# Optimization experiments

Hardware: AMD Instinct MI355X
Metric: run time of the kernel (lower is better)

The kernel has to match this reference:

```python
import jax, jax.numpy as jnp
import numpy as np

BATCH = 8
HIDDEN = 256          # per-head size == input channels
NUM_HEADS = 9
H_IMG = 48
W_IMG = 48


def make_R(w, h):
    """Relative-position feature tensor R[i,j,k,l] = [dx, dy, dx^2, dy^2, dx*dy]
    with dx = k - i, dy = l - j (matches torch.meshgrid indexing='ij')."""
    gx, gy = jnp.meshgrid(jnp.arange(w), jnp.arange(h), indexing='ij')
    grid = jnp.stack([gx, gy], axis=-1).astype(jnp.float32)        # (w,h,2)
    rel = grid[None, None, :, :, :] - grid[:, :, None, None, :]    # (w,h,w,h,2)
    return jnp.concatenate(
        [rel, rel ** 2, (rel[..., 0] * rel[..., 1])[..., None]], axis=-1
    )                                                              # (w,h,w,h,5)


def setup_inputs() -> dict:
    key = jax.random.key(0)
    k1, k2, k3, k4, k5 = jax.random.split(key, 5)
    hidden_states = jax.random.normal(k1, (BATCH, HIDDEN, H_IMG, W_IMG), dtype=jnp.float32)
    # init per module: centers ~ N(0, init_mu_std=2.0), spreads = 1 + N(0, 0.01)
    attention_centers = 2.0 * jax.random.normal(k2, (NUM_HEADS, 2), dtype=jnp.float32)
    attention_spreads = 1.0 + 0.01 * jax.random.normal(k3, (NUM_HEADS,), dtype=jnp.float32)
    value_w = 0.02 * jax.random.normal(k4, (HIDDEN, NUM_HEADS * HIDDEN), dtype=jnp.float32)
    value_b = 0.02 * jax.random.normal(k5, (HIDDEN,), dtype=jnp.float32)
    return {
        'hidden_states': hidden_states,
        'attention_centers': attention_centers,
        'attention_spreads': attention_spreads,
        'value_w': value_w,
        'value_b': value_b,
    }


def reference(hidden_states, attention_centers, attention_spreads, value_w, value_b):
    b, c, h, w = hidden_states.shape
    x = jnp.transpose(hidden_states, (0, 3, 2, 1))  # (b, w, h, c)

    # heads target vectors (isotropic gaussian): a = c = sigma^2, b = 0
    a = attention_spreads ** 2                       # (H,)
    mu1 = attention_centers[:, 0]
    mu2 = attention_centers[:, 1]
    # t_h = -1/2 * [-2 a mu1, -2 a mu2, a, a, 0] = [a mu1, a mu2, -a/2, -a/2, 0]
    u = jnp.stack([a * mu1, a * mu2, -0.5 * a, -0.5 * a, jnp.zeros_like(a)], axis=-1)  # (H,5)

    R = make_R(w, h)                                               # (w,h,w,h,5)
    scores = jnp.einsum('ijkld,hd->ijhkl', R, u)                   # (w,h,H,w,h)
    probs = jax.nn.softmax(scores.reshape(w, h, NUM_HEADS, -1), axis=-1)
    probs = probs.reshape(w, h, NUM_HEADS, w, h)
    # dropout is identity in eval mode

    vals = jnp.einsum('ijhkl,bkld->bijhd', probs, x)               # (b,w,h,H,c)
    vals = vals.reshape(b, w, h, NUM_HEADS * c)
    out = vals @ value_w.T + value_b                               # (b,w,h,hidden)
    out = jnp.transpose(out, (0, 3, 2, 1))                         # (b,hidden,h,w)
    return out, probs
```

## Files before the change

### kernel.cpp

```cpp
#include <hip/hip_runtime.h>
#include <cstdint>
#include <cstddef>

#define NHEAD 9
#define CHN   256
#define NB    8
#define WH    48
#define SS    2304
#define OUT0  4718592

typedef short bf16x8 __attribute__((ext_vector_type(8)));
typedef float f32x4  __attribute__((ext_vector_type(4)));

__device__ __forceinline__ float bf2f(unsigned int u16) {
    union { unsigned int i; float f; } v; v.i = u16 << 16; return v.f;
}
__device__ __forceinline__ unsigned short f2bf(float f) {
    union { float f; unsigned int i; } v; v.f = f;
    unsigned int x = v.i;
    unsigned int r = x + 0x7fffu + ((x >> 16) & 1u);
    return (unsigned short)(r >> 16);
}

__global__ __launch_bounds__(64) void k_pinit(const float* __restrict__ centers,
                                              const float* __restrict__ spreads,
                                              float* __restrict__ p1, float* __restrict__ p2,
                                              unsigned short* __restrict__ p1b,
                                              unsigned short* __restrict__ p2b) {
    int blk = blockIdx.x;
    int h = blk / 48, r = blk % 48;
    int lane = threadIdx.x;
    float a = spreads[h]; a = a * a;
    float mu1 = centers[2 * h + 0];
    float mu2 = centers[2 * h + 1];
    bool act = lane < 48;
    float dx = (float)(lane - r);
    float q  = -0.5f * a * dx * dx;
    float g1 = act ? (a * mu1 * dx + q) : -INFINITY;
    float g2 = act ? (a * mu2 * dx + q) : -INFINITY;
    float m1 = g1, m2 = g2;
    #pragma unroll
    for (int off = 32; off >= 1; off >>= 1) {
        m1 = fmaxf(m1, __shfl_xor(m1, off));
        m2 = fmaxf(m2, __shfl_xor(m2, off));
    }
    float e1 = act ? expf(g1 - m1) : 0.f;
    float e2 = act ? expf(g2 - m2) : 0.f;
    float s1 = e1, s2 = e2;
    #pragma unroll
    for (int off = 32; off >= 1; off >>= 1) {
        s1 += __shfl_xor(s1, off);
        s2 += __shfl_xor(s2, off);
    }
    float v1 = e1 / s1, v2 = e2 / s2;
    if (act) {
        p1[h * SS + r * 48 + lane] = v1;
        p2[h * SS + r * 48 + lane] = v2;
    }
    p1b[(h * 48 + r) * 64 + lane] = act ? f2bf(v1) : 0;
    p2b[(h * 48 + r) * 64 + lane] = act ? f2bf(v2) : 0;
}

__global__ __launch_bounds__(256) void k_hpack(const float* __restrict__ hs,
                                               unsigned short* __restrict__ hsb) {
    int bd = blockIdx.x;
    int t = threadIdx.x;
    const float* src = hs + (size_t)bd * SS;
    unsigned short* dst = hsb + (size_t)bd * 3072;
    for (int u = t; u < 384; u += 256) {
        int l = u >> 3, c8 = u & 7;
        uint4 o = {0u, 0u, 0u, 0u};
        if (c8 < 6) {
            const float* p = src + l * 48 + c8 * 8;
            float4 f0 = *(const float4*)p;
            float4 f1 = *(const float4*)(p + 4);
            o.x = (unsigned int)f2bf(f0.x) | ((unsigned int)f2bf(f0.y) << 16);
            o.y = (unsigned int)f2bf(f0.z) | ((unsigned int)f2bf(f0.w) << 16);
            o.z = (unsigned int)f2bf(f1.x) | ((unsigned int)f2bf(f1.y) << 16);
            o.w = (unsigned int)f2bf(f1.z) | ((unsigned int)f2bf(f1.w) << 16);
        }
        *(uint4*)(dst + l * 64 + c8 * 8) = o;
    }
}

__global__ __launch_bounds__(256, 2) void k_attn(const unsigned short* __restrict__ hsb,
                                                 const unsigned short* __restrict__ p1b,
                                                 const unsigned short* __restrict__ p2b,
                                                 unsigned short* __restrict__ AF) {
    __shared__ unsigned short Sbuf[4 * 3456];
    __shared__ unsigned short Vbuf[8 * 2304];

    int blk = blockIdx.x;
    int h = blk >> 8;
    int rem = blk & 255;
    int b = rem >> 5, od = rem & 31;
    int d0 = od * 8;
    int kb = h * 32 + od;

    int t = threadIdx.x;
    int lane = t & 63, wave = t >> 6;
    int l15 = lane & 15, quad = lane >> 4;

    const bf16x8* P1 = (const bf16x8*)(p1b + (size_t)h * 3072);
    const bf16x8* P2 = (const bf16x8*)(p2b + (size_t)h * 3072);
    bf16x8 pa[3][2], pb[3][2];
    #pragma unroll
    for (int tt = 0; tt < 3; ++tt)
        #pragma unroll
        for (int kt = 0; kt < 2; ++kt) {
            int u = (tt * 16 + l15) * 8 + kt * 4 + quad;
            pa[tt][kt] = P1[u];
            pb[tt][kt] = P2[u];
        }

    unsigned short* Sw = Sbuf + wave * 3456;
    for (int z = lane; z < 384; z += 64) {
        int row = z >> 3;
        *(unsigned int*)(Sw + row * 72 + 48 + ((z & 7) << 1)) = 0u;
    }

    for (int s = 0; s < 2; ++s) {
        int d = d0 + wave * 2 + s;
        int kk = wave * 2 + s;
        size_t bd = (size_t)b * 256 + d;
        const bf16x8* X = (const bf16x8*)(hsb + bd * 3072);

        bf16x8 bx[3][2];
        #pragma unroll
        for (int lt = 0; lt < 3; ++lt)
            #pragma unroll
            for (int kt = 0; kt < 2; ++kt)
                bx[lt][kt] = X[(lt * 16 + l15) * 8 + kt * 4 + quad];

        f32x4 a1[9];
        #pragma unroll
        for (int q = 0; q < 9; ++q) a1[q] = (f32x4){0.f, 0.f, 0.f, 0.f};
        #pragma unroll
        for (int it = 0; it < 3; ++it)
            #pragma unroll
            for (int lt = 0; lt < 3; ++lt) {
                a1[it * 3 + lt] = __builtin_amdgcn_mfma_f32_16x16x32_bf16(
                    pa[it][0], bx[lt][0], a1[it * 3 + lt], 0, 0, 0);
                a1[it * 3 + lt] = __builtin_amdgcn_mfma_f32_16x16x32_bf16(
                    pa[it][1], bx[lt][1], a1[it * 3 + lt], 0, 0, 0);
            }

        #pragma unroll
        for (int it = 0; it < 3; ++it)
            #pragma unroll
            for (int lt = 0; lt < 3; ++lt)
                #pragma unroll
                for (int r = 0; r < 4; ++r)
                    Sw[(it * 16 + quad * 4 + r) * 72 + lt * 16 + l15] =
                        f2bf(a1[it * 3 + lt][r]);

        bf16x8 a2f[3][2];
        #pragma unroll
        for (int it = 0; it < 3; ++it)
            #pragma unroll
            for (int kt = 0; kt < 2; ++kt)
                a2f[it][kt] = *(const bf16x8*)(Sw + (it * 16 + l15) * 72 + kt * 32 + quad * 8);

        f32x4 a2[9];
        #pragma unroll
        for (int q = 0; q < 9; ++q) a2[q] = (f32x4){0.f, 0.f, 0.f, 0.f};
        #pragma unroll
        for (int it = 0; it < 3; ++it)
            #pragma unroll
            for (int jt = 0; jt < 3; ++jt) {
                a2[it * 3 + jt] = __builtin_amdgcn_mfma_f32_16x16x32_bf16(
                    a2f[it][0], pb[jt][0], a2[it * 3 + jt], 0, 0, 0);
                a2[it * 3 + jt] = __builtin_amdgcn_mfma_f32_16x16x32_bf16(
                    a2f[it][1], pb[jt][1], a2[it * 3 + jt], 0, 0, 0);
            }

        #pragma unroll
        for (int it = 0; it < 3; ++it)
            #pragma unroll
            for (int jt = 0; jt < 3; ++jt) {
                f32x4 v = a2[it * 3 + jt];
                unsigned int lo = (unsigned int)f2bf(v[0]) | ((unsigned int)f2bf(v[1]) << 16);
                unsigned int hi = (unsigned int)f2bf(v[2]) | ((unsigned int)f2bf(v[3]) << 16);
                int m = (jt * 16 + l15) * 48 + it * 16 + quad * 4;
                uint2 u2; u2.x = lo; u2.y = hi;
                *(uint2*)(Vbuf + kk * 2304 + m) = u2;
            }
    }

    __syncthreads();

    const uint2* Vr = (const uint2*)Vbuf;
    uint4* AFq = (uint4*)AF;
    size_t abase = (size_t)(b * 288 + kb) * 2304;
    for (int g = t; g < 576; g += 256) {
        uint2 rk[8];
        #pragma unroll
        for (int kk = 0; kk < 8; ++kk) rk[kk] = Vr[kk * 576 + g];
        #pragma unroll
        for (int mi = 0; mi < 4; ++mi) {
            unsigned int sel = (mi & 1) ? 0x07060302u : 0x05040100u;
            uint4 o;
            if (mi < 2) {
                o.x = __builtin_amdgcn_perm(rk[1].x, rk[0].x, sel);
                o.y = __builtin_amdgcn_perm(rk[3].x, rk[2].x, sel);
                o.z = __builtin_amdgcn_perm(rk[5].x, rk[4].x, sel);
                o.w = __builtin_amdgcn_perm(rk[7].x, rk[6].x, sel);
            } else {
                o.x = __builtin_amdgcn_perm(rk[1].y, rk[0].y, sel);
                o.y = __builtin_amdgcn_perm(rk[3].y, rk[2].y, sel);
                o.z = __builtin_amdgcn_perm(rk[5].y, rk[4].y, sel);
                o.w = __builtin_amdgcn_perm(rk[7].y, rk[6].y, sel);
            }
            AFq[abase + g * 4 + mi] = o;
        }
    }
}

__global__ __launch_bounds__(256) void k_wpack(const float* __restrict__ Wv,
                                               unsigned short* __restrict__ WF) {
    int kb = blockIdx.x;
    int e  = threadIdx.x;
    const float* src = Wv + (size_t)e * 2304 + kb * 8;
    float4 f0 = *(const float4*)src;
    float4 f1 = *(const float4*)(src + 4);
    uint4 o;
    o.x = (unsigned int)f2bf(f0.x) | ((unsigned int)f2bf(f0.y) << 16);
    o.y = (unsigned int)f2bf(f0.z) | ((unsigned int)f2bf(f0.w) << 16);
    o.z = (unsigned int)f2bf(f1.x) | ((unsigned int)f2bf(f1.y) << 16);
    o.w = (unsigned int)f2bf(f1.z) | ((unsigned int)f2bf(f1.w) << 16);
    *(uint4*)(WF + ((size_t)kb * 256 + e) * 8) = o;
}

__global__ __launch_bounds__(256) void k_gemmC(const unsigned short* __restrict__ AF,
                                               const unsigned short* __restrict__ WF,
                                               const float* __restrict__ vb,
                                               float* __restrict__ out) {
    int blk = blockIdx.x;
    int b = blk / 72; int r = blk % 72; int mb = r >> 1; int nbk = r & 1;
    int t = threadIdx.x;
    int lane = t & 63, wave = t >> 6;
    int l15 = lane & 15, quad = lane >> 4;
    int wm = wave & 1, we = wave >> 1;
    int m0 = mb * 64 + wm * 32;
    int e0 = nbk * 128 + we * 64;

    const bf16x8* pa = (const bf16x8*)AF + (size_t)b * 288 * 2304
                       + (size_t)quad * 2304 + m0 + l15;
    const bf16x8* pw = (const bf16x8*)WF + (size_t)quad * 256 + e0 + l15;

    f32x4 acc[2][4];
    #pragma unroll
    for (int i = 0; i < 2; i++)
        #pragma unroll
        for (int j = 0; j < 4; j++) acc[i][j] = (f32x4){0.f, 0.f, 0.f, 0.f};

    bf16x8 a_cur[2], w_cur[4], a_nxt[2], w_nxt[4];
    a_cur[0] = pa[0];  a_cur[1] = pa[16];
    w_cur[0] = pw[0];  w_cur[1] = pw[16]; w_cur[2] = pw[32]; w_cur[3] = pw[48];

    for (int c = 0; c < 72; ++c) {
        if (c < 71) {
            a_nxt[0] = pa[9216];      a_nxt[1] = pa[9216 + 16];
            w_nxt[0] = pw[1024];      w_nxt[1] = pw[1024 + 16];
            w_nxt[2] = pw[1024 + 32]; w_nxt[3] = pw[1024 + 48];
        }
        #pragma unroll
        for (int tm = 0; tm < 2; ++tm)
            #pragma unroll
            for (int te = 0; te < 4; ++te)
                acc[tm][te] = __builtin_amdgcn_mfma_f32_16x16x32_bf16(
                    a_cur[tm], w_cur[te], acc[tm][te], 0, 0, 0);
        a_cur[0] = a_nxt[0]; a_cur[1] = a_nxt[1];
        w_cur[0] = w_nxt[0]; w_cur[1] = w_nxt[1]; w_cur[2] = w_nxt[2]; w_cur[3] = w_nxt[3];
        pa += 9216; pw += 1024;
    }

    size_t obase = (size_t)b * 589824;
    #pragma unroll
    for (int te = 0; te < 4; ++te) {
        int e = e0 + te * 16 + l15;
        float bias = vb[e];
        #pragma unroll
        for (int tm = 0; tm < 2; ++tm) {
            int m = m0 + tm * 16 + quad * 4;
            float4 v;
            v.x = acc[tm][te][0] + bias;
            v.y = acc[tm][te][1] + bias;
            v.z = acc[tm][te][2] + bias;
            v.w = acc[tm][te][3] + bias;
            *(float4*)(out + obase + (size_t)e * 2304 + m) = v;
        }
    }
}

__global__ __launch_bounds__(256) void k_probs(const float* __restrict__ p1,
                                               const float* __restrict__ p2,
                                               float* __restrict__ probs) {
    int blk = blockIdx.x;
    int h = blk % 9; int ij = blk / 9; int j = ij % 48; int i = ij / 48;
    __shared__ float p1row[48];
    __shared__ float4 p2row[12];
    int t = threadIdx.x;
    if (t < 48) p1row[t] = p1[(h * 48 + i) * 48 + t];
    else if (t < 60) p2row[t - 48] = ((const float4*)(p2 + (h * 48 + j) * 48))[t - 48];
    __syncthreads();
    float4* op = (float4*)(probs + (size_t)blk * SS);
    for (int idx = t; idx < 576; idx += 256) {
        int e4 = idx * 4;
        int k = e4 / 48, l = e4 % 48;
        float s = p1row[k];
        float4 qv = p2row[l >> 2];
        float4 v; v.x = s * qv.x; v.y = s * qv.y; v.z = s * qv.z; v.w = s * qv.w;
        op[idx] = v;
    }
}

extern "C" void kernel_launch(void* const* d_in, const int* in_sizes, int n_in,
                              void* d_out, int out_size, void* d_ws, size_t ws_size,
                              hipStream_t stream) {
    const float* hs      = (const float*)d_in[0];
    const float* centers = (const float*)d_in[1];
    const float* spreads = (const float*)d_in[2];
    const float* Wv      = (const float*)d_in[3];
    const float* vbias   = (const float*)d_in[4];

    float* out   = (float*)d_out;
    float* probs = out + OUT0;

    float* p1  = (float*)d_ws;
    float* p2  = p1 + 20736;
    unsigned short* p1b = (unsigned short*)(p2 + 20736);
    unsigned short* p2b = p1b + 27648;

    unsigned short* AF  = (unsigned short*)probs;
    unsigned short* WF  = AF + 42467328;
    unsigned short* hsb = WF + 589824;

    k_pinit<<<432, 64, 0, stream>>>(centers, spreads, p1, p2, p1b, p2b);
    k_hpack<<<2048, 256, 0, stream>>>(hs, hsb);
    k_wpack<<<288, 256, 0, stream>>>(Wv, WF);
    k_attn<<<2304, 256, 0, stream>>>(hsb, p1b, p2b, AF);
    k_gemmC<<<576, 256, 0, stream>>>(AF, WF, vbias, out);
    k_probs<<<20736, 256, 0, stream>>>(p1, p2, probs);
}
```

Measured before the change: 326.7 us.

## Merge prep kernels and co-schedule probs writes with attention kernel

Merges the three preprocessing kernels (softmax init, hidden-state pack, weight pack) into one launch with block-range dispatch. When the workspace is large enough, scratch buffers move out of the probs output region, so the probs-writing blocks can run in the same grid as the attention blocks. The probs writer now handles 8 rows per block and uses nontemporal stores. This cuts launch count and lets the bandwidth-heavy probs stores overlap compute-heavy MFMA work, at the cost of extra shared memory in the merged kernel and a fallback path when the workspace is small.

```diff
diff --git a/kernel.cpp b/kernel.cpp
--- a/kernel.cpp
+++ b/kernel.cpp
@@ -22,213 +22,242 @@
     return (unsigned short)(r >> 16);
 }
 
-__global__ __launch_bounds__(64) void k_pinit(const float* __restrict__ centers,
-                                              const float* __restrict__ spreads,
-                                              float* __restrict__ p1, float* __restrict__ p2,
-                                              unsigned short* __restrict__ p1b,
-                                              unsigned short* __restrict__ p2b) {
+__global__ __launch_bounds__(256) void k_pre(const float* __restrict__ centers,
+                                             const float* __restrict__ spreads,
+                                             const float* __restrict__ hs,
+                                             const float* __restrict__ Wv,
+                                             float* __restrict__ p1, float* __restrict__ p2,
+                                             unsigned short* __restrict__ p1b,
+                                             unsigned short* __restrict__ p2b,
+                                             unsigned short* __restrict__ hsb,
+                                             unsigned short* __restrict__ WF) {
     int blk = blockIdx.x;
-    int h = blk / 48, r = blk % 48;
-    int lane = threadIdx.x;
-    float a = spreads[h]; a = a * a;
-    float mu1 = centers[2 * h + 0];
-    float mu2 = centers[2 * h + 1];
-    bool act = lane < 48;
-    float dx = (float)(lane - r);
-    float q  = -0.5f * a * dx * dx;
-    float g1 = act ? (a * mu1 * dx + q) : -INFINITY;
-    float g2 = act ? (a * mu2 * dx + q) : -INFINITY;
-    float m1 = g1, m2 = g2;
-    #pragma unroll
-    for (int off = 32; off >= 1; off >>= 1) {
-        m1 = fmaxf(m1, __shfl_xor(m1, off));
-        m2 = fmaxf(m2, __shfl_xor(m2, off));
-    }
-    float e1 = act ? expf(g1 - m1) : 0.f;
-    float e2 = act ? expf(g2 - m2) : 0.f;
-    float s1 = e1, s2 = e2;
-    #pragma unroll
-    for (int off = 32; off >= 1; off >>= 1) {
-        s1 += __shfl_xor(s1, off);
-        s2 += __shfl_xor(s2, off);
-    }
-    float v1 = e1 / s1, v2 = e2 / s2;
-    if (act) {
-        p1[h * SS + r * 48 + lane] = v1;
-        p2[h * SS + r * 48 + lane] = v2;
-    }
-    p1b[(h * 48 + r) * 64 + lane] = act ? f2bf(v1) : 0;
-    p2b[(h * 48 + r) * 64 + lane] = act ? f2bf(v2) : 0;
-}
-
-__global__ __launch_bounds__(256) void k_hpack(const float* __restrict__ hs,
-                                               unsigned short* __restrict__ hsb) {
-    int bd = blockIdx.x;
     int t = threadIdx.x;
-    const float* src = hs + (size_t)bd * SS;
-    unsigned short* dst = hsb + (size_t)bd * 3072;
-    for (int u = t; u < 384; u += 256) {
-        int l = u >> 3, c8 = u & 7;
-        uint4 o = {0u, 0u, 0u, 0u};
-        if (c8 < 6) {
-            const float* p = src + l * 48 + c8 * 8;
-            float4 f0 = *(const float4*)p;
-            float4 f1 = *(const float4*)(p + 4);
-            o.x = (unsigned int)f2bf(f0.x) | ((unsigned int)f2bf(f0.y) << 16);
-            o.y = (unsigned int)f2bf(f0.z) | ((unsigned int)f2bf(f0.w) << 16);
-            o.z = (unsigned int)f2bf(f1.x) | ((unsigned int)f2bf(f1.y) << 16);
-            o.w = (unsigned int)f2bf(f1.z) | ((unsigned int)f2bf(f1.w) << 16);
-        }
-        *(uint4*)(dst + l * 64 + c8 * 8) = o;
-    }
-}
-
-__global__ __launch_bounds__(256, 2) void k_attn(const unsigned short* __restrict__ hsb,
-                                                 const unsigned short* __restrict__ p1b,
-                                                 const unsigned short* __restrict__ p2b,
-                                                 unsigned short* __restrict__ AF) {
-    __shared__ unsigned short Sbuf[4 * 3456];
-    __shared__ unsigned short Vbuf[8 * 2304];
-
+    if (blk < 108) {
+        int lane = t & 63, wave = t >> 6;
+        int ridx = blk * 4 + wave;
+        int h = ridx / 48, r = ridx % 48;
+        float a = spreads[h]; a = a * a;
+        float mu1 = centers[2 * h + 0];
+        float mu2 = centers[2 * h + 1];
+        bool act = lane < 48;
+        float dx = (float)(lane - r);
+        float q  = -0.5f * a * dx * dx;
+        float g1 = act ? (a * mu1 * dx + q) : -INFINITY;
+        float g2 = act ? (a * mu2 * dx + q) : -INFINITY;
+        float m1 = g1, m2 = g2;
+        #pragma unroll
+        for (int off = 32; off >= 1; off >>= 1) {
+            m1 = fmaxf(m1, __shfl_xor(m1, off));
+            m2 = fmaxf(m2, __shfl_xor(m2, off));
+        }
+        float e1 = act ? expf(g1 - m1) : 0.f;
+        float e2 = act ? expf(g2 - m2) : 0.f;
+        float s1 = e1, s2 = e2;
+        #pragma unroll
+        for (int off = 32; off >= 1; off >>= 1) {
+            s1 += __shfl_xor(s1, off);
+            s2 += __shfl_xor(s2, off);
+        }
+        float v1 = e1 / s1, v2 = e2 / s2;
+        if (act) {
+            p1[h * SS + r * 48 + lane] = v1;
+            p2[h * SS + r * 48 + lane] = v2;
+        }
+        p1b[(h * 48 + r) * 64 + lane] = act ? f2bf(v1) : 0;
+        p2b[(h * 48 + r) * 64 + lane] = act ? f2bf(v2) : 0;
+    } else if (blk < 396) {
+        int kb = blk - 108;
+        int e  = t;
+        const float* src = Wv + (size_t)e * 2304 + kb * 8;
+        float4 f0 = *(const float4*)src;
+        float4 f1 = *(const float4*)(src + 4);
+        uint4 o;
+        o.x = (unsigned int)f2bf(f0.x) | ((unsigned int)f2bf(f0.y) << 16);
+        o.y = (unsigned int)f2bf(f0.z) | ((unsigned int)f2bf(f0.w) << 16);
+        o.z = (unsigned int)f2bf(f1.x) | ((unsigned int)f2bf(f1.y) << 16);
+        o.w = (unsigned int)f2bf(f1.z) | ((unsigned int)f2bf(f1.w) << 16);
+        *(uint4*)(WF + ((size_t)kb * 256 + e) * 8) = o;
+    } else {
+        int bd = blk - 396;
+        const float* src = hs + (size_t)bd * SS;
+        unsigned short* dst = hsb + (size_t)bd * 3072;
+        for (int u = t; u < 384; u += 256) {
+            int l = u >> 3, c8 = u & 7;
+            uint4 o = {0u, 0u, 0u, 0u};
+            if (c8 < 6) {
+                const float* p = src + l * 48 + c8 * 8;
+                float4 f0 = *(const float4*)p;
+                float4 f1 = *(const float4*)(p + 4);
+                o.x = (unsigned int)f2bf(f0.x) | ((unsigned int)f2bf(f0.y) << 16);
+                o.y = (unsigned int)f2bf(f0.z) | ((unsigned int)f2bf(f0.w) << 16);
+                o.z = (unsigned int)f2bf(f1.x) | ((unsigned int)f2bf(f1.y) << 16);
+                o.w = (unsigned int)f2bf(f1.z) | ((unsigned int)f2bf(f1.w) << 16);
+            }
+            *(uint4*)(dst + l * 64 + c8 * 8) = o;
+        }
+    }
+}
+
+__global__ __launch_bounds__(256, 2) void k_attn_probs(const unsigned short* __restrict__ hsb,
+                                                       const unsigned short* __restrict__ p1b,
+                                                       const unsigned short* __restrict__ p2b,
+                                                       unsigned short* __restrict__ AF,
+                                                       const float* __restrict__ p1,
+                                                       const float* __restrict__ p2,
+                                                       float* __restrict__ probs,
+                                                       int nAttn) {
     int blk = blockIdx.x;
-    int h = blk >> 8;
-    int rem = blk & 255;
-    int b = rem >> 5, od = rem & 31;
-    int d0 = od * 8;
-    int kb = h * 32 + od;
-
     int t = threadIdx.x;
-    int lane = t & 63, wave = t >> 6;
-    int l15 = lane & 15, quad = lane >> 4;
-
-    const bf16x8* P1 = (const bf16x8*)(p1b + (size_t)h * 3072);
-    const bf16x8* P2 = (const bf16x8*)(p2b + (size_t)h * 3072);
-    bf16x8 pa[3][2], pb[3][2];
-    #pragma unroll
-    for (int tt = 0; tt < 3; ++tt)
-        #pragma unroll
-        for (int kt = 0; kt < 2; ++kt) {
-            int u = (tt * 16 + l15) * 8 + kt * 4 + quad;
-            pa[tt][kt] = P1[u];
-            pb[tt][kt] = P2[u];
-        }
-
-    unsigned short* Sw = Sbuf + wave * 3456;
-    for (int z = lane; z < 384; z += 64) {
-        int row = z >> 3;
-        *(unsigned int*)(Sw + row * 72 + 48 + ((z & 7) << 1)) = 0u;
-    }
-
-    for (int s = 0; s < 2; ++s) {
-        int d = d0 + wave * 2 + s;
-        int kk = wave * 2 + s;
-        size_t bd = (size_t)b * 256 + d;
-        const bf16x8* X = (const bf16x8*)(hsb + bd * 3072);
-
-        bf16x8 bx[3][2];
-        #pragma unroll
-        for (int lt = 0; lt < 3; ++lt)
-            #pragma unroll
-            for (int kt = 0; kt < 2; ++kt)
-                bx[lt][kt] = X[(lt * 16 + l15) * 8 + kt * 4 + quad];
-
-        f32x4 a1[9];
-        #pragma unroll
-        for (int q = 0; q < 9; ++q) a1[q] = (f32x4){0.f, 0.f, 0.f, 0.f};
-        #pragma unroll
-        for (int it = 0; it < 3; ++it)
-            #pragma unroll
-            for (int lt = 0; lt < 3; ++lt) {
-                a1[it * 3 + lt] = __builtin_amdgcn_mfma_f32_16x16x32_bf16(
-                    pa[it][0], bx[lt][0], a1[it * 3 + lt], 0, 0, 0);
-                a1[it * 3 + lt] = __builtin_amdgcn_mfma_f32_16x16x32_bf16(
-                    pa[it][1], bx[lt][1], a1[it * 3 + lt], 0, 0, 0);
+
+    if (blk < nAttn) {
+        __shared__ unsigned short Sbuf[4 * 3456];
+        __shared__ unsigned short Vbuf[8 * 2304];
+
+        int h = blk >> 8;
+        int rem = blk & 255;
+        int b = rem >> 5, od = rem & 31;
+        int d0 = od * 8;
+        int kb = h * 32 + od;
+
+        int lane = t & 63, wave = t >> 6;
+        int l15 = lane & 15, quad = lane >> 4;
+
+        const bf16x8* P1 = (const bf16x8*)(p1b + (size_t)h * 3072);
+        const bf16x8* P2 = (const bf16x8*)(p2b + (size_t)h * 3072);
+        bf16x8 pa[3][2], pb[3][2];
+        #pragma unroll
+        for (int tt = 0; tt < 3; ++tt)
+            #pragma unroll
+            for (int kt = 0; kt < 2; ++kt) {
+                int u = (tt * 16 + l15) * 8 + kt * 4 + quad;
+                pa[tt][kt] = P1[u];
+                pb[tt][kt] = P2[u];
             }
 
-        #pragma unroll
-        for (int it = 0; it < 3; ++it)
+        unsigned short* Sw = Sbuf + wave * 3456;
+        for (int z = lane; z < 384; z += 64) {
+            int row = z >> 3;
+            *(unsigned int*)(Sw + row * 72 + 48 + ((z & 7) << 1)) = 0u;
+        }
+
+        for (int s = 0; s < 2; ++s) {
+            int d = d0 + wave * 2 + s;
+            int kk = wave * 2 + s;
+            size_t bd = (size_t)b * 256 + d;
+            const bf16x8* X = (const bf16x8*)(hsb + bd * 3072);
+
+            bf16x8 bx[3][2];
             #pragma unroll
             for (int lt = 0; lt < 3; ++lt)
                 #pragma unroll
-                for (int r = 0; r < 4; ++r)
-                    Sw[(it * 16 + quad * 4 + r) * 72 + lt * 16 + l15] =
-                        f2bf(a1[it * 3 + lt][r]);
-
-        bf16x8 a2f[3][2];
-        #pragma unroll
-        for (int it = 0; it < 3; ++it)
-            #pragma unroll
-            for (int kt = 0; kt < 2; ++kt)
-                a2f[it][kt] = *(const bf16x8*)(Sw + (it * 16 + l15) * 72 + kt * 32 + quad * 8);
-
-        f32x4 a2[9];
-        #pragma unroll
-        for (int q = 0; q < 9; ++q) a2[q] = (f32x4){0.f, 0.f, 0.f, 0.f};
-        #pragma unroll
-        for (int it = 0; it < 3; ++it)
-            #pragma unroll
-            for (int jt = 0; jt < 3; ++jt) {
-                a2[it * 3 + jt] = __builtin_amdgcn_mfma_f32_16x16x32_bf16(
-                    a2f[it][0], pb[jt][0], a2[it * 3 + jt], 0, 0, 0);
-                a2[it * 3 + jt] = __builtin_amdgcn_mfma_f32_16x16x32_bf16(
-                    a2f[it][1], pb[jt][1], a2[it * 3 + jt], 0, 0, 0);
+                for (int kt = 0; kt < 2; ++kt)
+                    bx[lt][kt] = X[(lt * 16 + l15) * 8 + kt * 4 + quad];
+
+            f32x4 a1[9];
+            #pragma unroll
+            for (int q = 0; q < 9; ++q) a1[q] = (f32x4){0.f, 0.f, 0.f, 0.f};
+            #pragma unroll
+            for (int it = 0; it < 3; ++it)
+                #pragma unroll
+                for (int lt = 0; lt < 3; ++lt) {
+                    a1[it * 3 + lt] = __builtin_amdgcn_mfma_f32_16x16x32_bf16(
+                        pa[it][0], bx[lt][0], a1[it * 3 + lt], 0, 0, 0);
+                    a1[it * 3 + lt] = __builtin_amdgcn_mfma_f32_16x16x32_bf16(
+                        pa[it][1], bx[lt][1], a1[it * 3 + lt], 0, 0, 0);
+                }
+
+            #pragma unroll
+            for (int it = 0; it < 3; ++it)
+                #pragma unroll
+                for (int lt = 0; lt < 3; ++lt)
+                    #pragma unroll
+                    for (int r = 0; r < 4; ++r)
+                        Sw[(it * 16 + quad * 4 + r) * 72 + lt * 16 + l15] =
+                            f2bf(a1[it * 3 + lt][r]);
+
+            bf16x8 a2f[3][2];
+            #pragma unroll
+            for (int it = 0; it < 3; ++it)
+                #pragma unroll
+                for (int kt = 0; kt < 2; ++kt)
+                    a2f[it][kt] = *(const bf16x8*)(Sw + (it * 16 + l15) * 72 + kt * 32 + quad * 8);
+
+            f32x4 a2[9];
+            #pragma unroll
+            for (int q = 0; q < 9; ++q) a2[q] = (f32x4){0.f, 0.f, 0.f, 0.f};
+            #pragma unroll
+            for (int it = 0; it < 3; ++it)
+                #pragma unroll
+                for (int jt = 0; jt < 3; ++jt) {
+                    a2[it * 3 + jt] = __builtin_amdgcn_mfma_f32_16x16x32_bf16(
+                        a2f[it][0], pb[jt][0], a2[it * 3 + jt], 0, 0, 0);
+                    a2[it * 3 + jt] = __builtin_amdgcn_mfma_f32_16x16x32_bf16(
+                        a2f[it][1], pb[jt][1], a2[it * 3 + jt], 0, 0, 0);
+                }
+
+            #pragma unroll
+            for (int it = 0; it < 3; ++it)
+                #pragma unroll
+                for (int jt = 0; jt < 3; ++jt) {
+                    f32x4 v = a2[it * 3 + jt];
+                    unsigned int lo = (unsigned int)f2bf(v[0]) | ((unsigned int)f2bf(v[1]) << 16);
+                    unsigned int hi = (unsigned int)f2bf(v[2]) | ((unsigned int)f2bf(v[3]) << 16);
+                    int m = (jt * 16 + l15) * 48 + it * 16 + quad * 4;
+                    uint2 u2; u2.x = lo; u2.y = hi;
+                    *(uint2*)(Vbuf + kk * 2304 + m) = u2;
+                }
+        }
+
+        __syncthreads();
+
+        const uint2* Vr = (const uint2*)Vbuf;
+        uint4* AFq = (uint4*)AF;
+        size_t abase = (size_t)(b * 288 + kb) * 2304;
+        for (int g = t; g < 576; g += 256) {
+            uint2 rk[8];
+            #pragma unroll
+            for (int kk = 0; kk < 8; ++kk) rk[kk] = Vr[kk * 576 + g];
+            #pragma unroll
+            for (int mi = 0; mi < 4; ++mi) {
+                unsigned int sel = (mi & 1) ? 0x07060302u : 0x05040100u;
+                uint4 o;
+                if (mi < 2) {
+                    o.x = __builtin_amdgcn_perm(rk[1].x, rk[0].x, sel);
+                    o.y = __builtin_amdgcn_perm(rk[3].x, rk[2].x, sel);
+                    o.z = __builtin_amdgcn_perm(rk[5].x, rk[4].x, sel);
+                    o.w = __builtin_amdgcn_perm(rk[7].x, rk[6].x, sel);
+                } else {
+                    o.x = __builtin_amdgcn_perm(rk[1].y, rk[0].y, sel);
+                    o.y = __builtin_amdgcn_perm(rk[3].y, rk[2].y, sel);
+                    o.z = __builtin_amdgcn_perm(rk[5].y, rk[4].y, sel);
+                    o.w = __builtin_amdgcn_perm(rk[7].y, rk[6].y, sel);
+                }
+                AFq[abase + g * 4 + mi] = o;
             }
-
-        #pragma unroll
-        for (int it = 0; it < 3; ++it)
-            #pragma unroll
-            for (int jt = 0; jt < 3; ++jt) {
-                f32x4 v = a2[it * 3 + jt];
-                unsigned int lo = (unsigned int)f2bf(v[0]) | ((unsigned int)f2bf(v[1]) << 16);
-                unsigned int hi = (unsigned int)f2bf(v[2]) | ((unsigned int)f2bf(v[3]) << 16);
-                int m = (jt * 16 + l15) * 48 + it * 16 + quad * 4;
-                uint2 u2; u2.x = lo; u2.y = hi;
-                *(uint2*)(Vbuf + kk * 2304 + m) = u2;
+        }
+    } else {
+        int pb = blk - nAttn;
+        __shared__ float pr1[48];
+        __shared__ float4 pr2[12];
+        for (int tt = 0; tt < 8; ++tt) {
+            int idx = pb * 8 + tt;
+            int h = idx % 9; int ij = idx / 9; int j = ij % 48; int i = ij / 48;
+            __syncthreads();
+            if (t < 48) pr1[t] = p1[(h * 48 + i) * 48 + t];
+            else if (t < 60) pr2[t - 48] = ((const float4*)(p2 + (h * 48 + j) * 48))[t - 48];
+            __syncthreads();
+            f32x4* op = (f32x4*)(probs + (size_t)idx * SS);
+            for (int g = t; g < 576; g += 256) {
+                int e4 = g * 4;
+                int k = e4 / 48, l = e4 % 48;
+                float s = pr1[k];
+                float4 qv = pr2[l >> 2];
+                f32x4 v; v[0] = s * qv.x; v[1] = s * qv.y; v[2] = s * qv.z; v[3] = s * qv.w;
+                __builtin_nontemporal_store(v, op + g);
             }
-    }
-
-    __syncthreads();
-
-    const uint2* Vr = (const uint2*)Vbuf;
-    uint4* AFq = (uint4*)AF;
-    size_t abase = (size_t)(b * 288 + kb) * 2304;
-    for (int g = t; g < 576; g += 256) {
-        uint2 rk[8];
-        #pragma unroll
-        for (int kk = 0; kk < 8; ++kk) rk[kk] = Vr[kk * 576 + g];
-        #pragma unroll
-        for (int mi = 0; mi < 4; ++mi) {
-            unsigned int sel = (mi & 1) ? 0x07060302u : 0x05040100u;
-            uint4 o;
-            if (mi < 2) {
-                o.x = __builtin_amdgcn_perm(rk[1].x, rk[0].x, sel);
-                o.y = __builtin_amdgcn_perm(rk[3].x, rk[2].x, sel);
-                o.z = __builtin_amdgcn_perm(rk[5].x, rk[4].x, sel);
-                o.w = __builtin_amdgcn_perm(rk[7].x, rk[6].x, sel);
-            } else {
-                o.x = __builtin_amdgcn_perm(rk[1].y, rk[0].y, sel);
-                o.y = __builtin_amdgcn_perm(rk[3].y, rk[2].y, sel);
-                o.z = __builtin_amdgcn_perm(rk[5].y, rk[4].y, sel);
-                o.w = __builtin_amdgcn_perm(rk[7].y, rk[6].y, sel);
-            }
-            AFq[abase + g * 4 + mi] = o;
-        }
-    }
-}
-
-__global__ __launch_bounds__(256) void k_wpack(const float* __restrict__ Wv,
-                                               unsigned short* __restrict__ WF) {
-    int kb = blockIdx.x;
-    int e  = threadIdx.x;
-    const float* src = Wv + (size_t)e * 2304 + kb * 8;
-    float4 f0 = *(const float4*)src;
-    float4 f1 = *(const float4*)(src + 4);
-    uint4 o;
-    o.x = (unsigned int)f2bf(f0.x) | ((unsigned int)f2bf(f0.y) << 16);
-    o.y = (unsigned int)f2bf(f0.z) | ((unsigned int)f2bf(f0.w) << 16);
-    o.z = (unsigned int)f2bf(f1.x) | ((unsigned int)f2bf(f1.y) << 16);
-    o.w = (unsigned int)f2bf(f1.z) | ((unsigned int)f2bf(f1.w) << 16);
-    *(uint4*)(WF + ((size_t)kb * 256 + e) * 8) = o;
+        }
+    }
 }
 
 __global__ __launch_bounds__(256) void k_gemmC(const unsigned short* __restrict__ AF,
@@ -293,28 +322,6 @@
     }
 }
 
-__global__ __launch_bounds__(256) void k_probs(const float* __restrict__ p1,
-                                               const float* __restrict__ p2,
-                                               float* __restrict__ probs) {
-    int blk = blockIdx.x;
-    int h = blk % 9; int ij = blk / 9; int j = ij % 48; int i = ij / 48;
-    __shared__ float p1row[48];
-    __shared__ float4 p2row[12];
-    int t = threadIdx.x;
-    if (t < 48) p1row[t] = p1[(h * 48 + i) * 48 + t];
-    else if (t < 60) p2row[t - 48] = ((const float4*)(p2 + (h * 48 + j) * 48))[t - 48];
-    __syncthreads();
-    float4* op = (float4*)(probs + (size_t)blk * SS);
-    for (int idx = t; idx < 576; idx += 256) {
-        int e4 = idx * 4;
-        int k = e4 / 48, l = e4 % 48;
-        float s = p1row[k];
-        float4 qv = p2row[l >> 2];
-        float4 v; v.x = s * qv.x; v.y = s * qv.y; v.z = s * qv.z; v.w = s * qv.w;
-        op[idx] = v;
-    }
-}
-
 extern "C" void kernel_launch(void* const* d_in, const int* in_sizes, int n_in,
                               void* d_out, int out_size, void* d_ws, size_t ws_size,
                               hipStream_t stream) {
@@ -327,19 +334,37 @@
     float* out   = (float*)d_out;
     float* probs = out + OUT0;
 
-    float* p1  = (float*)d_ws;
-    float* p2  = p1 + 20736;
-    unsigned short* p1b = (unsigned short*)(p2 + 20736);
-    unsigned short* p2b = p1b + 27648;
-
-    unsigned short* AF  = (unsigned short*)probs;
-    unsigned short* WF  = AF + 42467328;
-    unsigned short* hsb = WF + 589824;
-
-    k_pinit<<<432, 64, 0, stream>>>(centers, spreads, p1, p2, p1b, p2b);
-    k_hpack<<<2048, 256, 0, stream>>>(hs, hsb);
-    k_wpack<<<288, 256, 0, stream>>>(Wv, WF);
-    k_attn<<<2304, 256, 0, stream>>>(hsb, p1b, p2b, AF);
-    k_gemmC<<<576, 256, 0, stream>>>(AF, WF, vbias, out);
-    k_probs<<<20736, 256, 0, stream>>>(p1, p2, probs);
-}
+    const size_t need = 98973696;
+    bool big = ws_size >= need;
+
+    unsigned short *AF, *WF, *hsb, *p1b, *p2b;
+    float *p1, *p2;
+    if (big) {
+        unsigned short* w = (unsigned short*)d_ws;
+        AF  = w;
+        WF  = AF + 42467328;
+        hsb = WF + 589824;
+        p1b = hsb + 6291456;
+        p2b = p1b + 27648;
+        p1  = (float*)(p2b + 27648);
+        p2  = p1 + 20736;
+    } else {
+        p1  = (float*)d_ws;
+        p2  = p1 + 20736;
+        p1b = (unsigned short*)(p2 + 20736);
+        p2b = p1b + 27648;
+        AF  = (unsigned short*)probs;
+        WF  = AF + 42467328;
+        hsb = WF + 589824;
+    }
+
+    k_pre<<<2444, 256, 0, stream>>>(centers, spreads, hs, Wv, p1, p2, p1b, p2b, hsb, WF);
+    if (big) {
+        k_attn_probs<<<2304 + 2592, 256, 0, stream>>>(hsb, p1b, p2b, AF, p1, p2, probs, 2304);
+        k_gemmC<<<576, 256, 0, stream>>>(AF, WF, vbias, out);
+    } else {
+        k_attn_probs<<<2304, 256, 0, stream>>>(hsb, p1b, p2b, AF, p1, p2, probs, 2304);
+        k_gemmC<<<576, 256, 0, stream>>>(AF, WF, vbias, out);
+        k_attn_probs<<<2592, 256, 0, stream>>>(hsb, p1b, p2b, AF, p1, p2, probs, 0);
+    }
+}
```

Result: no change. 327.1 us (+0.1%).
